# Optimization experiments

Measured on AMD Instinct MI355X. Metric: run time of the kernel, lower is better.

Reference implementation:

```python
import jax, jax.numpy as jnp
import numpy as np

N_NODES = 100000
N_EDGES = 1600000
IN_CH = 64
HID = 64


def setup_inputs() -> dict:
    key = jax.random.key(0)
    ks = jax.random.split(key, 6)
    x = jax.random.normal(ks[0], (N_NODES, IN_CH), dtype=jnp.float32)
    edge_index = jax.random.randint(ks[1], (2, N_EDGES), 0, N_NODES, dtype=jnp.int64)
    # Glorot-ish scaled weights
    W1 = jax.random.normal(ks[2], (IN_CH, HID), dtype=jnp.float32) / np.sqrt(IN_CH)
    b1 = jnp.zeros((HID,), dtype=jnp.float32)
    W2 = jax.random.normal(ks[3], (HID, HID), dtype=jnp.float32) / np.sqrt(HID)
    b2 = jnp.zeros((HID,), dtype=jnp.float32)
    Wl = jax.random.normal(ks[4], (HID, 1), dtype=jnp.float32) / np.sqrt(HID)
    bl = jnp.zeros((1,), dtype=jnp.float32)
    return {"x": x, "edge_index": edge_index, "W1": W1, "b1": b1,
            "W2": W2, "b2": b2, "Wl": Wl, "bl": bl}


def _gcn_conv(h, W, b, src, dst, norm, n_nodes):
    # GCNConv: linear transform, then sym-normalized neighborhood sum, then bias.
    h = h @ W                                  # [N, out]
    msg = h[src] * norm[:, None]               # [E+N, out] gather + scale
    agg = jax.ops.segment_sum(msg, dst, num_segments=n_nodes)  # scatter-add
    return agg + b


def reference(x, edge_index, W1, b1, W2, b2, Wl, bl):
    n = x.shape[0]
    self_loop = jnp.arange(n, dtype=edge_index.dtype)
    src = jnp.concatenate([edge_index[0], self_loop])  # message sources (x_j)
    dst = jnp.concatenate([edge_index[1], self_loop])  # aggregation targets
    # symmetric normalization deg^{-1/2}[src] * deg^{-1/2}[dst], deg incl. self-loops
    deg = jax.ops.segment_sum(jnp.ones_like(dst, dtype=x.dtype), dst, num_segments=n)
    dinv = jnp.where(deg > 0, jax.lax.rsqrt(jnp.maximum(deg, 1.0)), 0.0)
    norm = dinv[src] * dinv[dst]

    h = jax.nn.relu(_gcn_conv(x, W1, b1, src, dst, norm, n))
    # dropout is identity in eval mode
    h = _gcn_conv(h, W2, b2, src, dst, norm, n)
    return jax.nn.sigmoid(h @ Wl + bl)          # [N, 1]
```

## Files before the change

### kernel.cpp

```cpp
#include <hip/hip_runtime.h>
#include <hip/hip_fp16.h>

#define CH 64
#define NBUCK 1024
#define BSHIFT 7
#define BMASK 127
#define NBLK_P 512
#define RPMASK 0x1FFFFFu

typedef _Float16 f16x4 __attribute__((ext_vector_type(4)));
typedef float    f32x4 __attribute__((ext_vector_type(4)));


__global__ __launch_bounds__(256) void k_hist(const int* __restrict__ dst,
                                              int* __restrict__ blkhist, int E) {
    __shared__ int h[NBUCK];
    for (int i = threadIdx.x; i < NBUCK; i += blockDim.x) h[i] = 0;
    __syncthreads();
    int chunk = (E + NBLK_P - 1) / NBLK_P;
    int beg = blockIdx.x * chunk;
    int end = min(beg + chunk, E);
    for (int e = beg + threadIdx.x; e < end; e += blockDim.x)
        atomicAdd(&h[dst[e] >> BSHIFT], 1);
    __syncthreads();
    for (int i = threadIdx.x; i < NBUCK; i += blockDim.x)
        blkhist[blockIdx.x * NBUCK + i] = h[i];
}

__global__ __launch_bounds__(256) void k_bucketscan(const int* __restrict__ blkhist,
                                                    int* __restrict__ off_t,
                                                    int* __restrict__ tot) {
    int lane = threadIdx.x & 63;
    int t = (blockIdx.x * blockDim.x + threadIdx.x) >> 6;
    int v[8], pre[8];
    int sum = 0;
#pragma unroll
    for (int j = 0; j < 8; ++j) {
        v[j] = blkhist[(lane * 8 + j) * NBUCK + t];
        pre[j] = sum;
        sum += v[j];
    }
    int sc = sum;
#pragma unroll
    for (int o = 1; o < 64; o <<= 1) {
        int u = __shfl_up(sc, o, 64);
        if (lane >= o) sc += u;
    }
    int excl = sc - sum;
#pragma unroll
    for (int j = 0; j < 8; ++j)
        off_t[t * NBLK_P + lane * 8 + j] = excl + pre[j];
    if (lane == 63) tot[t] = sc;
}

__global__ __launch_bounds__(1024) void k_scantot(const int* __restrict__ tot,
                                                  int* __restrict__ bbase) {
    __shared__ int sh[NBUCK];
    int t = threadIdx.x;
    int v = tot[t];
    sh[t] = v;
    __syncthreads();
    for (int o = 1; o < NBUCK; o <<= 1) {
        int u = (t >= o) ? sh[t - o] : 0;
        __syncthreads();
        sh[t] += u;
        __syncthreads();
    }
    bbase[t] = sh[t] - v;
    if (t == NBUCK - 1) bbase[NBUCK] = sh[t];
}

__global__ __launch_bounds__(256) void k_partition(const int* __restrict__ src,
                                                   const int* __restrict__ dst,
                                                   const int* __restrict__ off_t,
                                                   const int* __restrict__ bbase,
                                                   unsigned int* __restrict__ ebuf, int E) {
    __shared__ int cur[NBUCK];
    for (int i = threadIdx.x; i < NBUCK; i += blockDim.x)
        cur[i] = bbase[i] + off_t[i * NBLK_P + blockIdx.x];
    __syncthreads();
    int chunk = (E + NBLK_P - 1) / NBLK_P;
    int beg = blockIdx.x * chunk;
    int end = min(beg + chunk, E);
    for (int e = beg + threadIdx.x; e < end; e += blockDim.x) {
        int s = src[e];
        int d = dst[e];
        int p = atomicAdd(&cur[d >> BSHIFT], 1);
        ebuf[p] = ((unsigned int)(d & BMASK) << 17) | (unsigned int)s;
    }
}

__global__ __launch_bounds__(256) void k_bucket_csr(const unsigned int* __restrict__ ebuf,
                                                    const int* __restrict__ bbase,
                                                    int* __restrict__ row_ptr,
                                                    float* __restrict__ dinv,
                                                    int* __restrict__ col, int n) {
    __shared__ int cnt[128];
    __shared__ int cur[128];
    __shared__ int sc[128];
    int t = threadIdx.x;
    int k = blockIdx.x;
    int e0 = bbase[k], e1 = bbase[k + 1];
    if (t < 128) cnt[t] = 0;
    __syncthreads();
    for (int e = e0 + t; e < e1; e += 256)
        atomicAdd(&cnt[ebuf[e] >> 17], 1);
    __syncthreads();
    int c = 0;
    if (t < 128) { c = cnt[t]; sc[t] = c; }
    __syncthreads();
    for (int o = 1; o < 128; o <<= 1) {
        int v = (t >= o && t < 128) ? sc[t - o] : 0;
        __syncthreads();
        if (t < 128) sc[t] += v;
        __syncthreads();
    }
    if (t < 128) {
        int excl = sc[t] - c;
        int prow = e0 + excl;
        int node = (k << BSHIFT) + t;
        if (node < n) {
            row_ptr[node] = prow | (c << 21);
            dinv[node] = rsqrtf((float)(c + 1));
        }
        cur[t] = prow;
    }
    __syncthreads();
    for (int e = e0 + t; e < e1; e += 256) {
        unsigned int u = ebuf[e];
        int p = atomicAdd(&cur[u >> 17], 1);
        col[p] = (int)(u & 0x1FFFFu);
    }
}


__global__ __launch_bounds__(256) void k_init(const float* __restrict__ W2,
                                              const float* __restrict__ Wl,
                                              float* __restrict__ wt,
                                              const float* __restrict__ W1,
                                              __half* __restrict__ wfrag) {
    if (threadIdx.x < 64) {
        int k = threadIdx.x;
        float s = 0.0f;
#pragma unroll 8
        for (int c = 0; c < CH; ++c) s = fmaf(W2[k * CH + c], Wl[c], s);
        wt[k] = s;
    }
    for (int idx = threadIdx.x; idx < 1024; idx += 256) {
        int f = idx >> 6;
        int l = idx & 63;
        int w4 = f >> 2, t = f & 3;
        int kb = w4 * 16 + 4 * (l >> 4);
        int c  = t * 16 + (l & 15);
#pragma unroll
        for (int b = 0; b < 4; ++b) {
            float wv = W1[(kb + b) * CH + c];
            __half hi = __float2half(wv);
            float lo = wv - __half2float(hi);
            wfrag[(size_t)f * 256 + l * 4 + b] = hi;
            wfrag[4096 + (size_t)f * 256 + l * 4 + b] = __float2half(lo);
        }
    }
}


__global__ __launch_bounds__(256) void k_gemm_mfma(const float* __restrict__ in,
                                                   const __half* __restrict__ wfrag,
                                                   const float* __restrict__ dinv,
                                                   __half* __restrict__ hs, int n) {
    if (blockIdx.x == 0 && threadIdx.x < CH)
        hs[(size_t)n * CH + threadIdx.x] = __float2half(0.0f);

    int lane = threadIdx.x & 63;
    int wid  = (blockIdx.x * blockDim.x + threadIdx.x) >> 6;
    int nw   = (gridDim.x * blockDim.x) >> 6;

    const f16x4* wf = (const f16x4*)wfrag;
    f16x4 wh[16], wl[16];
#pragma unroll
    for (int f = 0; f < 16; ++f) {
        wh[f] = wf[f * 64 + lane];
        wl[f] = wf[1024 + f * 64 + lane];
    }

    int r15 = lane & 15;
    int q   = lane >> 4;
    int ngrp = (n + 15) >> 4;

    for (int g = wid; g < ngrp; g += nw) {
        int base = g << 4;
        int arow = min(base + r15, n - 1);
        const float* ap = in + (size_t)arow * CH + 4 * q;

        f32x4 acc0 = {0.f, 0.f, 0.f, 0.f};
        f32x4 acc1 = {0.f, 0.f, 0.f, 0.f};
        f32x4 acc2 = {0.f, 0.f, 0.f, 0.f};
        f32x4 acc3 = {0.f, 0.f, 0.f, 0.f};

#pragma unroll
        for (int w4 = 0; w4 < 4; ++w4) {
            float4 xv = *(const float4*)(ap + w4 * 16);
            f16x4 ah, al;
            ah[0] = (_Float16)xv.x; al[0] = (_Float16)(xv.x - (float)ah[0]);
            ah[1] = (_Float16)xv.y; al[1] = (_Float16)(xv.y - (float)ah[1]);
            ah[2] = (_Float16)xv.z; al[2] = (_Float16)(xv.z - (float)ah[2]);
            ah[3] = (_Float16)xv.w; al[3] = (_Float16)(xv.w - (float)ah[3]);

            acc0 = __builtin_amdgcn_mfma_f32_16x16x16f16(ah, wh[w4 * 4 + 0], acc0, 0, 0, 0);
            acc1 = __builtin_amdgcn_mfma_f32_16x16x16f16(ah, wh[w4 * 4 + 1], acc1, 0, 0, 0);
            acc2 = __builtin_amdgcn_mfma_f32_16x16x16f16(ah, wh[w4 * 4 + 2], acc2, 0, 0, 0);
            acc3 = __builtin_amdgcn_mfma_f32_16x16x16f16(ah, wh[w4 * 4 + 3], acc3, 0, 0, 0);
            acc0 = __builtin_amdgcn_mfma_f32_16x16x16f16(al, wh[w4 * 4 + 0], acc0, 0, 0, 0);
            acc1 = __builtin_amdgcn_mfma_f32_16x16x16f16(al, wh[w4 * 4 + 1], acc1, 0, 0, 0);
            acc2 = __builtin_amdgcn_mfma_f32_16x16x16f16(al, wh[w4 * 4 + 2], acc2, 0, 0, 0);
            acc3 = __builtin_amdgcn_mfma_f32_16x16x16f16(al, wh[w4 * 4 + 3], acc3, 0, 0, 0);
            acc0 = __builtin_amdgcn_mfma_f32_16x16x16f16(ah, wl[w4 * 4 + 0], acc0, 0, 0, 0);
            acc1 = __builtin_amdgcn_mfma_f32_16x16x16f16(ah, wl[w4 * 4 + 1], acc1, 0, 0, 0);
            acc2 = __builtin_amdgcn_mfma_f32_16x16x16f16(ah, wl[w4 * 4 + 2], acc2, 0, 0, 0);
            acc3 = __builtin_amdgcn_mfma_f32_16x16x16f16(ah, wl[w4 * 4 + 3], acc3, 0, 0, 0);
        }

#pragma unroll
        for (int b = 0; b < 4; ++b) {
            int row = base + 4 * q + b;
            if (row < n) {
                float d = dinv[row];
                size_t o = (size_t)row * CH + r15;
                hs[o +  0] = __float2half(acc0[b] * d);
                hs[o + 16] = __float2half(acc1[b] * d);
                hs[o + 32] = __float2half(acc2[b] * d);
                hs[o + 48] = __float2half(acc3[b] * d);
            }
        }
    }
}


__global__ __launch_bounds__(256) void k_gather_gemm(const int* __restrict__ row_ptr,
                                                     const int* __restrict__ col,
                                                     const __half2* __restrict__ hs2,
                                                     const float* __restrict__ dinv,
                                                     const float* __restrict__ wt,
                                                     const float* __restrict__ bias,
                                                     float* __restrict__ z, int n) {
    int lane = threadIdx.x & 63;
    int l    = lane & 31;
    int g    = lane >> 5;
    int lg   = l & 7;
    int rg   = l >> 3;
    int wid  = (blockIdx.x * blockDim.x + threadIdx.x) >> 6;
    int nw   = (gridDim.x * blockDim.x) >> 6;

    float4 bi0 = ((const float4*)bias)[2 * lg];
    float4 bi1 = ((const float4*)bias)[2 * lg + 1];
    float4 wt0 = ((const float4*)wt)[2 * lg];
    float4 wt1 = ((const float4*)wt)[2 * lg + 1];

    int npairs = (n + 1) >> 1;
    int pr = wid;
    if (pr >= npairs) return;

    unsigned pkA = (unsigned)row_ptr[pr << 1];
    unsigned pkB = (unsigned)row_ptr[min((pr << 1) + 1, n - 1)];
    int cv = col[(int)((g ? pkB : pkA) & RPMASK) + l];

    for (; pr < npairs; pr += nw) {
        int a = pr << 1;
        bool hasB = (a + 1) < n;
        int begS = (int)((g ? pkB : pkA) & RPMASK);
        int degS = (int)((g ? pkB : pkA) >> 21);
        int degA = (int)(pkA >> 21), degB = (int)(pkB >> 21);
        int selfS = g ? (hasB ? a + 1 : a) : a;
        int mycv = cv;
        float dA = dinv[a];
        float dB = dinv[hasB ? a + 1 : a];

        float4 raw[8];
#pragma unroll
        for (int i = 0; i < 8; ++i) {
            int r = 4 * i + rg;
            int cr = __shfl(mycv, r, 32);
            int idx = (r < degS) ? cr : ((r == degS) ? selfS : n);
            raw[i] = *(const float4*)(hs2 + ((size_t)idx << 5) + (lg << 2));
        }

        int nxt = pr + nw;
        if (nxt < npairs) {
            int a1 = nxt << 1;
            pkA = (unsigned)row_ptr[a1];
            pkB = (unsigned)row_ptr[min(a1 + 1, n - 1)];
            cv = col[(int)((g ? pkB : pkA) & RPMASK) + l];
        }

        float2 a0 = make_float2(0.f, 0.f), a1 = make_float2(0.f, 0.f);
        float2 a2 = make_float2(0.f, 0.f), a3 = make_float2(0.f, 0.f);
#pragma unroll
        for (int i = 0; i < 8; ++i) {
            const __half2* hp = (const __half2*)&raw[i];
            float2 f0 = __half22float2(hp[0]);
            float2 f1 = __half22float2(hp[1]);
            float2 f2 = __half22float2(hp[2]);
            float2 f3 = __half22float2(hp[3]);
            a0.x += f0.x; a0.y += f0.y;
            a1.x += f1.x; a1.y += f1.y;
            a2.x += f2.x; a2.y += f2.y;
            a3.x += f3.x; a3.y += f3.y;
        }

        if (max(degA, degB) >= 32) {
            for (int r = 32 + rg; r <= degS; r += 4) {
                int idx = (r < degS) ? col[begS + r] : selfS;
                float4 rv = *(const float4*)(hs2 + ((size_t)idx << 5) + (lg << 2));
                const __half2* hp = (const __half2*)&rv;
                float2 f0 = __half22float2(hp[0]);
                float2 f1 = __half22float2(hp[1]);
                float2 f2 = __half22float2(hp[2]);
                float2 f3 = __half22float2(hp[3]);
                a0.x += f0.x; a0.y += f0.y;
                a1.x += f1.x; a1.y += f1.y;
                a2.x += f2.x; a2.y += f2.y;
                a3.x += f3.x; a3.y += f3.y;
            }
        }

        a0.x += __shfl_xor(a0.x, 8, 64);  a0.y += __shfl_xor(a0.y, 8, 64);
        a1.x += __shfl_xor(a1.x, 8, 64);  a1.y += __shfl_xor(a1.y, 8, 64);
        a2.x += __shfl_xor(a2.x, 8, 64);  a2.y += __shfl_xor(a2.y, 8, 64);
        a3.x += __shfl_xor(a3.x, 8, 64);  a3.y += __shfl_xor(a3.y, 8, 64);
        a0.x += __shfl_xor(a0.x, 16, 64); a0.y += __shfl_xor(a0.y, 16, 64);
        a1.x += __shfl_xor(a1.x, 16, 64); a1.y += __shfl_xor(a1.y, 16, 64);
        a2.x += __shfl_xor(a2.x, 16, 64); a2.y += __shfl_xor(a2.y, 16, 64);
        a3.x += __shfl_xor(a3.x, 16, 64); a3.y += __shfl_xor(a3.y, 16, 64);

        float d = g ? dB : dA;
        float p;
        {
            float v;
            v = fmaxf(fmaf(a0.x, d, bi0.x), 0.0f); p  = v * wt0.x;
            v = fmaxf(fmaf(a0.y, d, bi0.y), 0.0f); p = fmaf(v, wt0.y, p);
            v = fmaxf(fmaf(a1.x, d, bi0.z), 0.0f); p = fmaf(v, wt0.z, p);
            v = fmaxf(fmaf(a1.y, d, bi0.w), 0.0f); p = fmaf(v, wt0.w, p);
            v = fmaxf(fmaf(a2.x, d, bi1.x), 0.0f); p = fmaf(v, wt1.x, p);
            v = fmaxf(fmaf(a2.y, d, bi1.y), 0.0f); p = fmaf(v, wt1.y, p);
            v = fmaxf(fmaf(a3.x, d, bi1.z), 0.0f); p = fmaf(v, wt1.z, p);
            v = fmaxf(fmaf(a3.y, d, bi1.w), 0.0f); p = fmaf(v, wt1.w, p);
        }
        p += __shfl_xor(p, 1, 64);
        p += __shfl_xor(p, 2, 64);
        p += __shfl_xor(p, 4, 64);
        p *= d;
        if (l == 0 && (g == 0 || hasB)) z[a + g] = p;
    }
}


__global__ __launch_bounds__(256) void k_head(const int* __restrict__ row_ptr,
                                              const int* __restrict__ col,
                                              const float* __restrict__ z,
                                              const float* __restrict__ dinv,
                                              const float* __restrict__ b2,
                                              const float* __restrict__ Wl,
                                              const float* __restrict__ bl,
                                              float* __restrict__ out, int n) {
    int lane = threadIdx.x & 63;
    float c0 = b2[lane] * Wl[lane];
#pragma unroll
    for (int o = 32; o > 0; o >>= 1) c0 += __shfl_xor(c0, o, 64);
    c0 += bl[0];

    int tid = blockIdx.x * blockDim.x + threadIdx.x;
    int st  = gridDim.x * blockDim.x;
    int n4  = n << 2;
    for (int q = tid; q < n4; q += st) {
        int node = q >> 2;
        int sub  = q & 3;
        unsigned pk = (unsigned)row_ptr[node];
        int beg = (int)(pk & RPMASK);
        int deg = (int)(pk >> 21);
        float s0 = (sub == 0) ? z[node] : 0.0f;
        float s1 = 0.0f;
        int e = sub;
        for (; e + 4 < deg; e += 8) {
            s0 += z[col[beg + e]];
            s1 += z[col[beg + e + 4]];
        }
        if (e < deg) s0 += z[col[beg + e]];
        float s = s0 + s1;
        s += __shfl_xor(s, 1, 64);
        s += __shfl_xor(s, 2, 64);
        if (sub == 0) {
            float v = dinv[node] * s + c0;
            out[node] = 1.0f / (1.0f + expf(-v));
        }
    }
}


extern "C" void kernel_launch(void* const* d_in, const int* in_sizes, int n_in,
                              void* d_out, int out_size, void* d_ws, size_t ws_size,
                              hipStream_t stream) {
    const float* x   = (const float*)d_in[0];
    const int*   ei  = (const int*)d_in[1];
    const float* W1  = (const float*)d_in[2];
    const float* b1  = (const float*)d_in[3];
    const float* W2  = (const float*)d_in[4];
    const float* b2  = (const float*)d_in[5];
    const float* Wl  = (const float*)d_in[6];
    const float* bl  = (const float*)d_in[7];
    float*       out = (float*)d_out;

    const int N = in_sizes[0] / CH;
    const int E = in_sizes[1] / 2;
    const int* src = ei;
    const int* dst = ei + E;

    const size_t Npad = ((size_t)N + 511) & ~(size_t)511;
    const size_t Epad = ((size_t)E + 511) & ~(size_t)511;
    const size_t COLSZ = Epad + 512;

    float* z        = (float*)d_ws;
    float* dinv     = z + Npad;
    int*   row_ptr  = (int*)(dinv + Npad);
    float* wt       = (float*)(row_ptr + Npad);
    __half* wfrag   = (__half*)(wt + 512);
    int*   col      = (int*)(wfrag + 8192);
    unsigned int* ebuf = (unsigned int*)(col + COLSZ);
    int*   blkhist  = (int*)(ebuf + Epad);
    int*   off_t    = blkhist + (size_t)NBLK_P * NBUCK;
    int*   bbase    = off_t + (size_t)NBLK_P * NBUCK;
    int*   tot      = bbase + NBUCK + 64;
    __half* A       = (__half*)ebuf;

    const int TB = 256;
    const int GRID = 2048;
    const int NB_USED = (N + BMASK) >> BSHIFT;

    k_init<<<1, TB, 0, stream>>>(W2, Wl, wt, W1, wfrag);

    k_hist<<<NBLK_P, TB, 0, stream>>>(dst, blkhist, E);
    k_bucketscan<<<NBUCK * 64 / TB, TB, 0, stream>>>(blkhist, off_t, tot);
    k_scantot<<<1, NBUCK, 0, stream>>>(tot, bbase);
    k_partition<<<NBLK_P, TB, 0, stream>>>(src, dst, off_t, bbase, ebuf, E);
    k_bucket_csr<<<NB_USED, TB, 0, stream>>>(ebuf, bbase, row_ptr, dinv, col, N);

    k_gemm_mfma<<<784, TB, 0, stream>>>(x, wfrag, dinv, A, N);

    k_gather_gemm<<<2 * GRID, TB, 0, stream>>>(row_ptr, col, (const __half2*)A, dinv,
                                               wt, b1, z, N);

    k_head<<<((N << 2) + TB - 1) / TB, TB, 0, stream>>>(row_ptr, col, z, dinv,
                                                        b2, Wl, bl, out, N);
}
```

Baseline: 186.5 us.

## Fuse weight prep and bucket-total scan into neighbouring kernels, widen head gather

```diff
diff --git a/kernel.cpp b/kernel.cpp
--- a/kernel.cpp
+++ b/kernel.cpp
@@ -13,7 +13,12 @@
 
 
 __global__ __launch_bounds__(256) void k_hist(const int* __restrict__ dst,
-                                              int* __restrict__ blkhist, int E) {
+                                              int* __restrict__ blkhist, int E,
+                                              const float* __restrict__ W2,
+                                              const float* __restrict__ Wl,
+                                              float* __restrict__ wt,
+                                              const float* __restrict__ W1,
+                                              __half* __restrict__ wfrag) {
     __shared__ int h[NBUCK];
     for (int i = threadIdx.x; i < NBUCK; i += blockDim.x) h[i] = 0;
     __syncthreads();
@@ -25,6 +30,31 @@
     __syncthreads();
     for (int i = threadIdx.x; i < NBUCK; i += blockDim.x)
         blkhist[blockIdx.x * NBUCK + i] = h[i];
+
+    if (blockIdx.x == 0) {
+        if (threadIdx.x < 64) {
+            int k = threadIdx.x;
+            float s = 0.0f;
+#pragma unroll 8
+            for (int c = 0; c < CH; ++c) s = fmaf(W2[k * CH + c], Wl[c], s);
+            wt[k] = s;
+        }
+        for (int idx = threadIdx.x; idx < 1024; idx += 256) {
+            int f = idx >> 6;
+            int l = idx & 63;
+            int w4 = f >> 2, t = f & 3;
+            int kb = w4 * 16 + 4 * (l >> 4);
+            int c  = t * 16 + (l & 15);
+#pragma unroll
+            for (int b = 0; b < 4; ++b) {
+                float wv = W1[(kb + b) * CH + c];
+                __half hi = __float2half(wv);
+                float lo = wv - __half2float(hi);
+                wfrag[(size_t)f * 256 + l * 4 + b] = hi;
+                wfrag[4096 + (size_t)f * 256 + l * 4 + b] = __float2half(lo);
+            }
+        }
+    }
 }
 
 __global__ __launch_bounds__(256) void k_bucketscan(const int* __restrict__ blkhist,
@@ -53,57 +83,65 @@
     if (lane == 63) tot[t] = sc;
 }
 
-__global__ __launch_bounds__(1024) void k_scantot(const int* __restrict__ tot,
-                                                  int* __restrict__ bbase) {
-    __shared__ int sh[NBUCK];
-    int t = threadIdx.x;
-    int v = tot[t];
-    sh[t] = v;
-    __syncthreads();
-    for (int o = 1; o < NBUCK; o <<= 1) {
-        int u = (t >= o) ? sh[t - o] : 0;
-        __syncthreads();
-        sh[t] += u;
-        __syncthreads();
-    }
-    bbase[t] = sh[t] - v;
-    if (t == NBUCK - 1) bbase[NBUCK] = sh[t];
-}
-
 __global__ __launch_bounds__(256) void k_partition(const int* __restrict__ src,
                                                    const int* __restrict__ dst,
                                                    const int* __restrict__ off_t,
-                                                   const int* __restrict__ bbase,
+                                                   const int* __restrict__ tot,
                                                    unsigned int* __restrict__ ebuf, int E) {
     __shared__ int cur[NBUCK];
-    for (int i = threadIdx.x; i < NBUCK; i += blockDim.x)
-        cur[i] = bbase[i] + off_t[i * NBLK_P + blockIdx.x];
+    __shared__ int psum[256];
+    int t = threadIdx.x;
+    int b = blockIdx.x;
+    int4 tv = *(const int4*)(tot + 4 * t);
+    int s = tv.x + tv.y + tv.z + tv.w;
+    psum[t] = s;
+    __syncthreads();
+    for (int o = 1; o < 256; o <<= 1) {
+        int u = (t >= o) ? psum[t - o] : 0;
+        __syncthreads();
+        psum[t] += u;
+        __syncthreads();
+    }
+    int base = psum[t] - s;
+    cur[4 * t + 0] = base                       + off_t[(4 * t + 0) * NBLK_P + b];
+    cur[4 * t + 1] = base + tv.x                + off_t[(4 * t + 1) * NBLK_P + b];
+    cur[4 * t + 2] = base + tv.x + tv.y         + off_t[(4 * t + 2) * NBLK_P + b];
+    cur[4 * t + 3] = base + tv.x + tv.y + tv.z  + off_t[(4 * t + 3) * NBLK_P + b];
     __syncthreads();
     int chunk = (E + NBLK_P - 1) / NBLK_P;
-    int beg = blockIdx.x * chunk;
+    int beg = b * chunk;
     int end = min(beg + chunk, E);
     for (int e = beg + threadIdx.x; e < end; e += blockDim.x) {
-        int s = src[e];
+        int sv = src[e];
         int d = dst[e];
         int p = atomicAdd(&cur[d >> BSHIFT], 1);
-        ebuf[p] = ((unsigned int)(d & BMASK) << 17) | (unsigned int)s;
-    }
-}
-
-__global__ __launch_bounds__(256) void k_bucket_csr(const unsigned int* __restrict__ ebuf,
-                                                    const int* __restrict__ bbase,
+        ebuf[p] = ((unsigned int)(d & BMASK) << 17) | (unsigned int)sv;
+    }
+}
+
+__global__ __launch_bounds__(512) void k_bucket_csr(const unsigned int* __restrict__ ebuf,
+                                                    const int* __restrict__ tot,
                                                     int* __restrict__ row_ptr,
                                                     float* __restrict__ dinv,
                                                     int* __restrict__ col, int n) {
     __shared__ int cnt[128];
     __shared__ int cur[128];
     __shared__ int sc[128];
+    __shared__ int rsum[512];
     int t = threadIdx.x;
     int k = blockIdx.x;
-    int e0 = bbase[k], e1 = bbase[k + 1];
+    int part = 0;
+    for (int i = t; i < k; i += 512) part += tot[i];
+    rsum[t] = part;
     if (t < 128) cnt[t] = 0;
     __syncthreads();
-    for (int e = e0 + t; e < e1; e += 256)
+    for (int o = 256; o > 0; o >>= 1) {
+        if (t < o) rsum[t] += rsum[t + o];
+        __syncthreads();
+    }
+    int e0 = rsum[0];
+    int e1 = e0 + tot[k];
+    for (int e = e0 + t; e < e1; e += 512)
         atomicAdd(&cnt[ebuf[e] >> 17], 1);
     __syncthreads();
     int c = 0;
@@ -126,40 +164,10 @@
         cur[t] = prow;
     }
     __syncthreads();
-    for (int e = e0 + t; e < e1; e += 256) {
+    for (int e = e0 + t; e < e1; e += 512) {
         unsigned int u = ebuf[e];
         int p = atomicAdd(&cur[u >> 17], 1);
         col[p] = (int)(u & 0x1FFFFu);
-    }
-}
-
-
-__global__ __launch_bounds__(256) void k_init(const float* __restrict__ W2,
-                                              const float* __restrict__ Wl,
-                                              float* __restrict__ wt,
-                                              const float* __restrict__ W1,
-                                              __half* __restrict__ wfrag) {
-    if (threadIdx.x < 64) {
-        int k = threadIdx.x;
-        float s = 0.0f;
-#pragma unroll 8
-        for (int c = 0; c < CH; ++c) s = fmaf(W2[k * CH + c], Wl[c], s);
-        wt[k] = s;
-    }
-    for (int idx = threadIdx.x; idx < 1024; idx += 256) {
-        int f = idx >> 6;
-        int l = idx & 63;
-        int w4 = f >> 2, t = f & 3;
-        int kb = w4 * 16 + 4 * (l >> 4);
-        int c  = t * 16 + (l & 15);
-#pragma unroll
-        for (int b = 0; b < 4; ++b) {
-            float wv = W1[(kb + b) * CH + c];
-            __half hi = __float2half(wv);
-            float lo = wv - __half2float(hi);
-            wfrag[(size_t)f * 256 + l * 4 + b] = hi;
-            wfrag[4096 + (size_t)f * 256 + l * 4 + b] = __float2half(lo);
-        }
     }
 }
 
@@ -370,24 +378,18 @@
 
     int tid = blockIdx.x * blockDim.x + threadIdx.x;
     int st  = gridDim.x * blockDim.x;
-    int n4  = n << 2;
-    for (int q = tid; q < n4; q += st) {
-        int node = q >> 2;
-        int sub  = q & 3;
+    int n8  = n << 3;
+    for (int q = tid; q < n8; q += st) {
+        int node = q >> 3;
+        int sub  = q & 7;
         unsigned pk = (unsigned)row_ptr[node];
         int beg = (int)(pk & RPMASK);
         int deg = (int)(pk >> 21);
-        float s0 = (sub == 0) ? z[node] : 0.0f;
-        float s1 = 0.0f;
-        int e = sub;
-        for (; e + 4 < deg; e += 8) {
-            s0 += z[col[beg + e]];
-            s1 += z[col[beg + e + 4]];
-        }
-        if (e < deg) s0 += z[col[beg + e]];
-        float s = s0 + s1;
+        float s = (sub == 0) ? z[node] : 0.0f;
+        for (int e = sub; e < deg; e += 8) s += z[col[beg + e]];
         s += __shfl_xor(s, 1, 64);
         s += __shfl_xor(s, 2, 64);
+        s += __shfl_xor(s, 4, 64);
         if (sub == 0) {
             float v = dinv[node] * s + c0;
             out[node] = 1.0f / (1.0f + expf(-v));
@@ -427,27 +429,23 @@
     unsigned int* ebuf = (unsigned int*)(col + COLSZ);
     int*   blkhist  = (int*)(ebuf + Epad);
     int*   off_t    = blkhist + (size_t)NBLK_P * NBUCK;
-    int*   bbase    = off_t + (size_t)NBLK_P * NBUCK;
-    int*   tot      = bbase + NBUCK + 64;
+    int*   tot      = off_t + (size_t)NBLK_P * NBUCK;
     __half* A       = (__half*)ebuf;
 
     const int TB = 256;
     const int GRID = 2048;
     const int NB_USED = (N + BMASK) >> BSHIFT;
 
-    k_init<<<1, TB, 0, stream>>>(W2, Wl, wt, W1, wfrag);
-
-    k_hist<<<NBLK_P, TB, 0, stream>>>(dst, blkhist, E);
+    k_hist<<<NBLK_P, TB, 0, stream>>>(dst, blkhist, E, W2, Wl, wt, W1, wfrag);
     k_bucketscan<<<NBUCK * 64 / TB, TB, 0, stream>>>(blkhist, off_t, tot);
-    k_scantot<<<1, NBUCK, 0, stream>>>(tot, bbase);
-    k_partition<<<NBLK_P, TB, 0, stream>>>(src, dst, off_t, bbase, ebuf, E);
-    k_bucket_csr<<<NB_USED, TB, 0, stream>>>(ebuf, bbase, row_ptr, dinv, col, N);
+    k_partition<<<NBLK_P, TB, 0, stream>>>(src, dst, off_t, tot, ebuf, E);
+    k_bucket_csr<<<NB_USED, 512, 0, stream>>>(ebuf, tot, row_ptr, dinv, col, N);
 
     k_gemm_mfma<<<784, TB, 0, stream>>>(x, wfrag, dinv, A, N);
 
     k_gather_gemm<<<2 * GRID, TB, 0, stream>>>(row_ptr, col, (const __half2*)A, dinv,
                                                wt, b1, z, N);
 
-    k_head<<<((N << 2) + TB - 1) / TB, TB, 0, stream>>>(row_ptr, col, z, dinv,
+    k_head<<<((N << 3) + TB - 1) / TB, TB, 0, stream>>>(row_ptr, col, z, dinv,
                                                         b2, Wl, bl, out, N);
 }
```

Result: no change. 188.1 us (+0.9%).
